# Optimization experiments

Measured on AMD Instinct MI355X. Metric: run time of the kernel, lower is better.

Reference implementation:

```python
import jax, jax.numpy as jnp
import numpy as np

B, S, E, H, NE, TOPK = 8, 1024, 768, 12, 8, 2
F = 4 * E
DH = E // H

def _ln(x, g, b, eps=1e-5):
    m = jnp.mean(x, axis=-1, keepdims=True)
    v = jnp.mean((x - m) ** 2, axis=-1, keepdims=True)
    return (x - m) / jnp.sqrt(v + eps) * g + b

def _expert(x, lg, lb, w1, b1, w2, b2):
    # Expert: LayerNorm -> Linear(E,4E) -> GELU(exact) -> Linear(4E,E); dropout is identity in eval
    h = _ln(x, lg, lb)
    h = jax.nn.gelu(h @ w1.T + b1, approximate=False)
    return h @ w2.T + b2

def setup_inputs():
    key = jax.random.key(0)
    ks = jax.random.split(key, 16)
    rn = lambda k, shape, s=0.02: jax.random.normal(k, shape, jnp.float32) * s
    return {
        'x': jax.random.normal(ks[0], (B, S, E), jnp.float32),
        'modality_type': jax.random.randint(ks[1], (B, S), 0, 2).astype(jnp.int32),
        'norm1_g': jnp.ones((E,), jnp.float32), 'norm1_b': jnp.zeros((E,), jnp.float32),
        'norm2_g': jnp.ones((E,), jnp.float32), 'norm2_b': jnp.zeros((E,), jnp.float32),
        'in_proj_w': rn(ks[2], (3 * E, E)), 'in_proj_b': jnp.zeros((3 * E,), jnp.float32),
        'out_proj_w': rn(ks[3], (E, E)), 'out_proj_b': jnp.zeros((E,), jnp.float32),
        'router_w': rn(ks[4], (NE, E)), 'router_b': jnp.zeros((NE,), jnp.float32),
        'spec_ln_g': jnp.ones((3, E), jnp.float32), 'spec_ln_b': jnp.zeros((3, E), jnp.float32),
        'spec_w1': rn(ks[5], (3, F, E)), 'spec_b1': jnp.zeros((3, F), jnp.float32),
        'spec_w2': rn(ks[6], (3, E, F)), 'spec_b2': jnp.zeros((3, E), jnp.float32),
        'gen_ln_g': jnp.ones((NE, E), jnp.float32), 'gen_ln_b': jnp.zeros((NE, E), jnp.float32),
        'gen_w1': rn(ks[7], (NE, F, E)), 'gen_b1': jnp.zeros((NE, F), jnp.float32),
        'gen_w2': rn(ks[8], (NE, E, F)), 'gen_b2': jnp.zeros((NE, E), jnp.float32),
    }

def _forward(x, modality_type, norm1_g, norm1_b, norm2_g, norm2_b, in_proj_w, in_proj_b,
             out_proj_w, out_proj_b, router_w, router_b,
             spec_ln_g, spec_ln_b, spec_w1, spec_b1, spec_w2, spec_b2,
             gen_ln_g, gen_ln_b, gen_w1, gen_b1, gen_w2, gen_b2):
    # --- self-attention block (pre-norm + residual), matches nn.MultiheadAttention ---
    residual = x
    xn = _ln(x, norm1_g, norm1_b)
    qkv = xn @ in_proj_w.T + in_proj_b                          # [B,S,3E]
    q, k, v = jnp.split(qkv, 3, axis=-1)
    q = q.reshape(B, S, H, DH); k = k.reshape(B, S, H, DH); v = v.reshape(B, S, H, DH)
    scores = jnp.einsum('bqhd,bkhd->bhqk', q, k) / jnp.sqrt(jnp.float32(DH))
    attn = jax.nn.softmax(scores, axis=-1)
    ctx = jnp.einsum('bhqk,bkhd->bqhd', attn, v).reshape(B, S, E)
    x = residual + (ctx @ out_proj_w.T + out_proj_b)

    # --- MoE block (pre-norm + residual) ---
    residual = x
    xn = _ln(x, norm2_g, norm2_b)
    expert_out = _expert(xn, spec_ln_g[0], spec_ln_b[0], spec_w1[0], spec_b1[0], spec_w2[0], spec_b2[0])
    # modality experts: vision on tokens with type==0, text on type==1 (not a fusion layer)
    vmask = (modality_type == 0).astype(xn.dtype)[..., None]
    tmask = (modality_type == 1).astype(xn.dtype)[..., None]
    expert_out = expert_out + vmask * _expert(xn, spec_ln_g[1], spec_ln_b[1], spec_w1[1], spec_b1[1], spec_w2[1], spec_b2[1])
    expert_out = expert_out + tmask * _expert(xn, spec_ln_g[2], spec_ln_b[2], spec_w1[2], spec_b1[2], spec_w2[2], spec_b2[2])

    # --- router: softmax -> top_k -> renormalize over top_k ---
    logits = xn @ router_w.T + router_b                         # [B,S,NE]
    probs = jax.nn.softmax(logits, axis=-1)
    topk_probs, topk_idx = jax.lax.top_k(probs, TOPK)
    topk_w = jax.nn.softmax(topk_probs, axis=-1)                # [B,S,TOPK]

    # --- dispatch/combine: per-expert combine coefficient; experts are per-token so
    # dense masked compute is mathematically identical to the torch gather/scatter loop ---
    for e in range(NE):
        coef = jnp.sum(topk_w * (topk_idx == e), axis=-1)[..., None]   # [B,S,1]
        expert_out = expert_out + coef * _expert(xn, gen_ln_g[e], gen_ln_b[e], gen_w1[e], gen_b1[e], gen_w2[e], gen_b2[e])

    return residual + expert_out

def reference(x, modality_type, norm1_g, norm1_b, norm2_g, norm2_b, in_proj_w, in_proj_b,
              out_proj_w, out_proj_b, router_w, router_b,
              spec_ln_g, spec_ln_b, spec_w1, spec_b1, spec_w2, spec_b2,
              gen_ln_g, gen_ln_b, gen_w1, gen_b1, gen_w2, gen_b2):
    return _forward(x, modality_type, norm1_g, norm1_b, norm2_g, norm2_b, in_proj_w, in_proj_b,
                    out_proj_w, out_proj_b, router_w, router_b,
                    spec_ln_g, spec_ln_b, spec_w1, spec_b1, spec_w2, spec_b2,
                    gen_ln_g, gen_ln_b, gen_w1, gen_b1, gen_w2, gen_b2)
```

## Files before the change

kernel.cpp:

```cpp
#include <hip/hip_runtime.h>
#include <cstdint>

#define NTOK 8192
#define EDIM 768
#define FDIM 3072

using bf16x8 = __attribute__((ext_vector_type(8))) __bf16;
using f32x4  = __attribute__((ext_vector_type(4))) float;

__device__ __forceinline__ float b2f(ushort u){ union{uint32_t i; float f;} v; v.i = ((uint32_t)u)<<16; return v.f; }
__device__ __forceinline__ ushort f2b(float f){ union{float f; uint32_t i;} v; v.f=f; uint32_t r = v.i + 0x7fffu + ((v.i>>16)&1u); return (ushort)(r>>16); }
__device__ __forceinline__ float gelu_f(float v){
  float c = v*(1.5957691216f + 0.0713548162726f*v*v);
  return v / (1.f + __expf(-c));
}
__device__ __forceinline__ void gload16(const ushort* g, ushort* l){
  __builtin_amdgcn_global_load_lds((const __attribute__((address_space(1))) void*)g,
                                   (__attribute__((address_space(3))) void*)l, 16, 0, 0);
}

__global__ __launch_bounds__(256) void conv_w(const float* w0,const float* w1,const float* w2,
                                              const float* w3,const float* w4,const float* w5,
                                              const float* slg, const float* glg,
                                              ushort* pool)
{
  size_t idx4 = (size_t)blockIdx.x*256 + threadIdx.x;
  size_t e = idx4*4;
  const float* src; size_t base; int region;
  if      (e <  1769472u){src=w0;base=0;        region=0;}
  else if (e <  2359296u){src=w1;base=1769472u; region=1;}
  else if (e <  9437184u){src=w2;base=2359296u; region=2;}
  else if (e < 16515072u){src=w3;base=9437184u; region=3;}
  else if (e < 35389440u){src=w4;base=16515072u;region=4;}
  else                   {src=w5;base=35389440u;region=5;}
  size_t within = e - base;
  f32x4 f = *(const f32x4*)(src + within);
  if (region==2){
    int ex = (int)(within/2359296u); int col = (int)(within%768u);
    f32x4 g = *(const f32x4*)(slg + ex*768 + col);
    f[0]*=g[0]; f[1]*=g[1]; f[2]*=g[2]; f[3]*=g[3];
  } else if (region==4){
    int ex = (int)(within/2359296u); int col = (int)(within%768u);
    f32x4 g = *(const f32x4*)(glg + ex*768 + col);
    f[0]*=g[0]; f[1]*=g[1]; f[2]*=g[2]; f[3]*=g[3];
  }
  ushort4 u; u.x=f2b(f[0]); u.y=f2b(f[1]); u.z=f2b(f[2]); u.w=f2b(f[3]);
  *(ushort4*)(pool+e) = u;
}

__global__ __launch_bounds__(256) void b1fold_k(const float* __restrict__ sw1, const float* __restrict__ gw1,
                                                const float* __restrict__ sb1, const float* __restrict__ gb1,
                                                const float* __restrict__ slb, const float* __restrict__ glb,
                                                float* __restrict__ b1p)
{
  int j = blockIdx.x*4 + (threadIdx.x>>6);
  int lane = threadIdx.x & 63;
  int je = j / FDIM, f = j % FDIM;
  const float* wrow = (je<3) ? sw1 + ((size_t)je*FDIM + f)*EDIM : gw1 + ((size_t)(je-3)*FDIM + f)*EDIM;
  const float* lb   = (je<3) ? slb + (size_t)je*EDIM : glb + (size_t)(je-3)*EDIM;
  float s = 0.f;
  #pragma unroll
  for (int i=0;i<12;i++){ int d = lane + 64*i; s += wrow[d]*lb[d]; }
  #pragma unroll
  for (int o=32;o>0;o>>=1) s += __shfl_xor(s,o);
  if (lane==0){
    float base = (je<3) ? sb1[je*FDIM+f] : gb1[(je-3)*FDIM+f];
    b1p[j] = base + s;
  }
}

__global__ __launch_bounds__(256) void out_init(const float* __restrict__ x, const float* __restrict__ bo,
                                                float* __restrict__ out)
{
  size_t i = ((size_t)blockIdx.x*256 + threadIdx.x)*4;
  int col = (int)(i % EDIM);
  f32x4 xv = *(const f32x4*)(x+i);
  f32x4 bv = *(const f32x4*)(bo+col);
  f32x4 r = { xv[0]+bv[0], xv[1]+bv[1], xv[2]+bv[2], xv[3]+bv[3] };
  *(f32x4*)(out+i) = r;
}

__global__ __launch_bounds__(256) void ln1_k(const float* __restrict__ x, const float* __restrict__ g,
                                             const float* __restrict__ b, ushort* __restrict__ out)
{
  int w = blockIdx.x*4 + (threadIdx.x>>6);
  int lane = threadIdx.x & 63;
  const float* xr = x + (size_t)w*EDIM;
  float v[12]; float s=0.f, s2=0.f;
  #pragma unroll
  for (int i=0;i<12;i++){ v[i]=xr[lane+64*i]; s+=v[i]; s2+=v[i]*v[i]; }
  #pragma unroll
  for (int o=32;o>0;o>>=1){ s += __shfl_xor(s,o); s2 += __shfl_xor(s2,o); }
  float mu = s*(1.f/768.f);
  float rs = rsqrtf(s2*(1.f/768.f) - mu*mu + 1e-5f);
  ushort* op = out + (size_t)w*EDIM;
  #pragma unroll
  for (int i=0;i<12;i++){ int d=lane+64*i; op[d] = f2b((v[i]-mu)*rs*g[d] + b[d]); }
}

__global__ __launch_bounds__(256) void lnr_k(const float* __restrict__ x1, const float* __restrict__ g2,
                                             const float* __restrict__ b2, const float* __restrict__ rw,
                                             const float* __restrict__ rbv,
                                             ushort* __restrict__ z, float* __restrict__ coef)
{
  int w = blockIdx.x*4 + (threadIdx.x>>6);
  int lane = threadIdx.x & 63;
  const float* xr = x1 + (size_t)w*EDIM;
  float v[12]; float s=0.f, s2=0.f;
  #pragma unroll
  for (int i=0;i<12;i++){ v[i]=xr[lane+64*i]; s+=v[i]; s2+=v[i]*v[i]; }
  #pragma unroll
  for (int o=32;o>0;o>>=1){ s += __shfl_xor(s,o); s2 += __shfl_xor(s2,o); }
  float mu = s*(1.f/768.f);
  float rs = rsqrtf(s2*(1.f/768.f) - mu*mu + 1e-5f);
  float xn[12]; s=0.f; s2=0.f;
  #pragma unroll
  for (int i=0;i<12;i++){ int d=lane+64*i; xn[i]=(v[i]-mu)*rs*g2[d]+b2[d]; s+=xn[i]; s2+=xn[i]*xn[i]; }
  float pl[8] = {0.f,0.f,0.f,0.f,0.f,0.f,0.f,0.f};
  #pragma unroll
  for (int i=0;i<12;i++){
    int d=lane+64*i; float xv=xn[i];
    #pragma unroll
    for (int e=0;e<8;e++) pl[e] += xv * rw[e*EDIM + d];
  }
  #pragma unroll
  for (int o=32;o>0;o>>=1){ s += __shfl_xor(s,o); s2 += __shfl_xor(s2,o); }
  float mu2 = s*(1.f/768.f);
  float rs2 = rsqrtf(s2*(1.f/768.f) - mu2*mu2 + 1e-5f);
  ushort* op = z + (size_t)w*EDIM;
  #pragma unroll
  for (int i=0;i<12;i++){ int d=lane+64*i; op[d] = f2b((xn[i]-mu2)*rs2); }
  #pragma unroll
  for (int e=0;e<8;e++){
    #pragma unroll
    for (int o=32;o>0;o>>=1) pl[e] += __shfl_xor(pl[e], o);
  }
  float lgt[8]; float mx = -1e30f;
  #pragma unroll
  for (int e=0;e<8;e++){ lgt[e]=pl[e]+rbv[e]; mx = fmaxf(mx, lgt[e]); }
  float p[8]; float den=0.f;
  #pragma unroll
  for (int e=0;e<8;e++){ p[e]=__expf(lgt[e]-mx); den+=p[e]; }
  float inv = 1.f/den;
  #pragma unroll
  for (int e=0;e<8;e++) p[e]*=inv;
  int i1=0;
  #pragma unroll
  for (int e=1;e<8;e++) if (p[e]>p[i1]) i1=e;
  int i2=(i1==0)?1:0;
  #pragma unroll
  for (int e=0;e<8;e++){ if (e==i1) continue; if (p[e]>p[i2]) i2=e; }
  float w1 = 1.f/(1.f+__expf(p[i2]-p[i1]));
  float w2 = 1.f - w1;
  if (lane < 8){
    float c = (lane==i1)? w1 : ((lane==i2)? w2 : 0.f);
    coef[(size_t)w*8 + lane] = c;
  }
}

__global__ __launch_bounds__(256) void build_lists(const int* __restrict__ mt, const float* __restrict__ coef,
                                                   ushort* __restrict__ lists, ushort* __restrict__ inv,
                                                   int* __restrict__ cnt)
{
  const int job = blockIdx.x;
  ushort* list = lists + (size_t)job*NTOK;
  __shared__ int wsum[4];
  int base = 0;
  const int lane = threadIdx.x & 63, wv = threadIdx.x >> 6;
  for (int c0=0; c0<NTOK; c0+=256){
    int t = c0 + threadIdx.x;
    bool flag;
    if (job==0)      flag = (mt[t]==0);
    else if (job==1) flag = (mt[t]==1);
    else             flag = (coef[(size_t)t*8 + (job-2)] != 0.0f);
    unsigned long long bal = __ballot(flag);
    int pre = __popcll(bal & ((1ull<<lane)-1ull));
    if (lane==0) wsum[wv] = __popcll(bal);
    __syncthreads();
    int off = base + pre;
    for (int k=0;k<wv;k++) off += wsum[k];
    int tot = wsum[0]+wsum[1]+wsum[2]+wsum[3];
    if (flag){ list[off] = (ushort)t; inv[(size_t)job*NTOK + t] = (ushort)off; }
    base += tot;
    __syncthreads();
  }
  if (threadIdx.x==0){ cnt[job+1] = base; if (job==0) cnt[0] = NTOK; }
}

__global__ __launch_bounds__(256) void gather_k(const float* __restrict__ coef, const int* __restrict__ mt,
                                                const ushort* __restrict__ inv, const int* __restrict__ cnt,
                                                const ushort* __restrict__ outC, float* __restrict__ out,
                                                int phase)
{
  int t = blockIdx.x*4 + (threadIdx.x>>6);
  int lane = threadIdx.x & 63;
  int r0, r1; float c0=1.f, c1=1.f;
  if (phase==0){
    r0 = t;
    int m = mt[t];
    r1 = NTOK + (m ? cnt[1] : 0) + (int)inv[(size_t)m*NTOK + t];
  } else {
    int found=0; int rr[2]={0,0}; float cc[2]={0.f,0.f}; int base=0;
    #pragma unroll
    for (int e=0;e<8;e++){
      float ce = coef[(size_t)t*8+e];
      if (ce != 0.f && found<2){ rr[found]=base+(int)inv[(size_t)(2+e)*NTOK + t]; cc[found]=ce; found++; }
      base += cnt[3+e];
    }
    r0=rr[0]; r1=rr[1]; c0=cc[0]; c1=cc[1];
  }
  const ushort* pa = outC + (size_t)r0*EDIM;
  const ushort* pb = outC + (size_t)r1*EDIM;
  float* po = out + (size_t)t*EDIM;
  #pragma unroll
  for (int i=0;i<3;i++){
    int d = lane*4 + 256*i;
    ushort4 ua = *(const ushort4*)(pa+d);
    ushort4 ub = *(const ushort4*)(pb+d);
    f32x4 o = *(f32x4*)(po+d);
    o[0] += c0*b2f(ua.x) + c1*b2f(ub.x);
    o[1] += c0*b2f(ua.y) + c1*b2f(ub.y);
    o[2] += c0*b2f(ua.z) + c1*b2f(ub.z);
    o[3] += c0*b2f(ua.w) + c1*b2f(ub.w);
    *(f32x4*)(po+d) = o;
  }
}

struct GemmArgs {
  const ushort* A; const ushort* B;
  const float* bias;
  ushort* outBF;
  int K, ldc;
};

__global__ __launch_bounds__(256) void gemm_k(GemmArgs g)
{
  const int mb = blockIdx.x, nb = blockIdx.y;
  __shared__ __align__(1024) ushort As[128*32];
  __shared__ __align__(1024) ushort Bs[128*32];
  const int tid = threadIdx.x;
  const int lane = tid & 63, w = tid >> 6;
  const int seg = lane & 3;
  const int lrow = w*16 + (lane>>2);
  const int p = (lane>>3)&3;
  ushort* ldsA0 = As + (size_t)w*512;
  ushort* ldsA1 = As + (size_t)(w+4)*512;
  ushort* ldsB0 = Bs + (size_t)w*512;
  ushort* ldsB1 = Bs + (size_t)(w+4)*512;
  const int KK = g.K;
  const ushort* pA0 = g.A + (size_t)(mb*128 + lrow)*KK + (seg^p)*8;
  const ushort* pA1 = pA0 + (size_t)64*KK;
  const ushort* pB0 = g.B + (size_t)(nb*128 + lrow)*KK + (seg^p)*8;
  const ushort* pB1 = pB0 + (size_t)64*KK;
  const int nst = KK >> 5;
  f32x4 acc[4][4];
  #pragma unroll
  for (int m=0;m<4;m++)
    #pragma unroll
    for (int n=0;n<4;n++) acc[m][n] = (f32x4){0.f,0.f,0.f,0.f};
  const int fr = lane & 15, fq = lane >> 4;
  const int pr = (fr>>1)&3;
  const int so = (fq^pr)*8;
  const int rb_ = (w>>1)*64, cb_ = (w&1)*64;
  for (int kt=0; kt<nst; ++kt){
    __syncthreads();
    gload16(pA0, ldsA0); gload16(pA1, ldsA1);
    gload16(pB0, ldsB0); gload16(pB1, ldsB1);
    pA0 += 32; pA1 += 32; pB0 += 32; pB1 += 32;
    __syncthreads();
    bf16x8 af[4], bfr[4];
    #pragma unroll
    for (int m=0;m<4;m++) af[m]  = *(const bf16x8*)&As[(rb_ + m*16 + fr)*32 + so];
    #pragma unroll
    for (int n=0;n<4;n++) bfr[n] = *(const bf16x8*)&Bs[(cb_ + n*16 + fr)*32 + so];
    #pragma unroll
    for (int m=0;m<4;m++)
      #pragma unroll
      for (int n=0;n<4;n++)
        acc[m][n] = __builtin_amdgcn_mfma_f32_16x16x32_bf16(af[m], bfr[n], acc[m][n], 0, 0, 0);
  }
  #pragma unroll
  for (int m=0;m<4;m++){
    #pragma unroll
    for (int j=0;j<4;j++){
      const int row = mb*128 + rb_ + m*16 + fq*4 + j;
      #pragma unroll
      for (int n=0;n<4;n++){
        const int col = nb*128 + cb_ + n*16 + fr;
        g.outBF[(size_t)row*g.ldc + col] = f2b(acc[m][n][j] + g.bias[col]);
      }
    }
  }
}

struct FArgs {
  const ushort* z; ushort* hidden; const ushort* ctx; const ushort* wo;
  float* out; ushort* outC;
  const ushort* lists; const ushort* inv; const int* cnt; const float* coef;
  const ushort* sw1; const ushort* gw1; const ushort* sw2; const ushort* gw2;
  const float* b1p; const float* sb2; const float* gb2;
  int jobBase; int compact; int mode;
};

__device__ __forceinline__ size_t job_hoff(const FArgs& a, int job){
  size_t h = 0;
  if (a.compact){
    if (job==1) h = NTOK;
    else if (job==2) h = NTOK + (size_t)a.cnt[1];
    else if (job>=3){ for (int k=3;k<job;k++) h += (size_t)a.cnt[k]; }
  }
  return h;
}

__global__ __launch_bounds__(256) void ffn1_k(FArgs a)
{
  const int job = a.jobBase + blockIdx.z;
  const int cntj = (job==0) ? NTOK : a.cnt[job];
  const int mb = blockIdx.x, nb = blockIdx.y;
  if (mb*128 >= cntj) return;
  const ushort* list = (job==0) ? nullptr : a.lists + (size_t)(job-1)*NTOK;
  const ushort* B = (job<3) ? a.sw1+(size_t)job*FDIM*EDIM : a.gw1+(size_t)(job-3)*FDIM*EDIM;
  const float* bias = a.b1p + (size_t)job*FDIM;
  const size_t hoff = job_hoff(a, job);
  __shared__ __align__(1024) ushort As[128*32];
  __shared__ __align__(1024) ushort Bs[128*32];
  const int tid = threadIdx.x;
  const int lane = tid & 63, w = tid >> 6;
  const int seg = lane & 3;
  const int lrow = w*16 + (lane>>2);
  const int p = (lane>>3)&3;
  ushort* ldsA0 = As + (size_t)w*512;
  ushort* ldsA1 = As + (size_t)(w+4)*512;
  ushort* ldsB0 = Bs + (size_t)w*512;
  ushort* ldsB1 = Bs + (size_t)(w+4)*512;
  const int r0 = mb*128 + lrow, r1 = r0 + 64;
  const int tA0 = list ? (int)list[min(r0,cntj-1)] : min(r0,cntj-1);
  const int tA1 = list ? (int)list[min(r1,cntj-1)] : min(r1,cntj-1);
  const ushort* pA0 = a.z + (size_t)tA0*EDIM + (seg^p)*8;
  const ushort* pA1 = a.z + (size_t)tA1*EDIM + (seg^p)*8;
  const ushort* pB0 = B + (size_t)(nb*128 + lrow)*EDIM + (seg^p)*8;
  const ushort* pB1 = pB0 + (size_t)64*EDIM;
  f32x4 acc[4][4];
  #pragma unroll
  for (int m=0;m<4;m++)
    #pragma unroll
    for (int n=0;n<4;n++) acc[m][n] = (f32x4){0.f,0.f,0.f,0.f};
  const int fr = lane & 15, fq = lane >> 4;
  const int pr = (fr>>1)&3;
  const int so = (fq^pr)*8;
  const int rb_ = (w>>1)*64, cb_ = (w&1)*64;
  for (int kt=0; kt<24; ++kt){
    __syncthreads();
    gload16(pA0, ldsA0); gload16(pA1, ldsA1);
    gload16(pB0, ldsB0); gload16(pB1, ldsB1);
    pA0 += 32; pA1 += 32; pB0 += 32; pB1 += 32;
    __syncthreads();
    bf16x8 af[4], bfr[4];
    #pragma unroll
    for (int m=0;m<4;m++) af[m]  = *(const bf16x8*)&As[(rb_ + m*16 + fr)*32 + so];
    #pragma unroll
    for (int n=0;n<4;n++) bfr[n] = *(const bf16x8*)&Bs[(cb_ + n*16 + fr)*32 + so];
    #pragma unroll
    for (int m=0;m<4;m++)
      #pragma unroll
      for (int n=0;n<4;n++)
        acc[m][n] = __builtin_amdgcn_mfma_f32_16x16x32_bf16(af[m], bfr[n], acc[m][n], 0, 0, 0);
  }
  #pragma unroll
  for (int m=0;m<4;m++){
    #pragma unroll
    for (int j=0;j<4;j++){
      const int row = mb*128 + rb_ + m*16 + fq*4 + j;
      if (row < cntj){
        #pragma unroll
        for (int n=0;n<4;n++){
          const int col = nb*128 + cb_ + n*16 + fr;
          a.hidden[(hoff+row)*FDIM + col] = f2b(gelu_f(acc[m][n][j] + bias[col]));
        }
      }
    }
  }
}

__global__ __launch_bounds__(256) void ffn2_k(FArgs a)
{
  const bool op = (a.jobBase < 0);
  const int job = op ? -1 : a.jobBase + blockIdx.z;
  const int cntj = op ? NTOK : ((job==0) ? NTOK : a.cnt[job]);
  const int mb = blockIdx.x, nb = blockIdx.y;
  if (mb*64 >= cntj) return;
  const ushort* list = (op || job==0) ? nullptr : a.lists + (size_t)(job-1)*NTOK;
  const ushort* Abase; int lda; const ushort* B; const float* bias = nullptr;
  const float* coefp = nullptr; int eidx = 0;
  if (op){ Abase = a.ctx; lda = EDIM; B = a.wo; }
  else {
    lda = FDIM;
    Abase = a.hidden + job_hoff(a, job)*FDIM;
    if (job<3){ B=a.sw2+(size_t)job*(size_t)EDIM*FDIM; bias=a.sb2+(size_t)job*EDIM; }
    else { eidx=job-3; B=a.gw2+(size_t)eidx*(size_t)EDIM*FDIM; bias=a.gb2+(size_t)eidx*EDIM; coefp=a.coef; }
  }
  const size_t hoff = op ? 0 : job_hoff(a, job);
  const int nst = lda >> 5;
  __shared__ __align__(1024) ushort As[64*32];
  __shared__ __align__(1024) ushort Bs[128*32];
  const int tid = threadIdx.x;
  const int lane = tid & 63, w = tid >> 6;
  const int seg = lane & 3;
  const int lrow = w*16 + (lane>>2);
  const int p = (lane>>3)&3;
  ushort* ldsA  = As + (size_t)w*512;
  ushort* ldsB0 = Bs + (size_t)w*512;
  ushort* ldsB1 = Bs + (size_t)(w+4)*512;
  const int r0 = mb*64 + lrow;
  const ushort* pA  = Abase + (size_t)min(r0,cntj-1)*lda + (seg^p)*8;
  const ushort* pB0 = B + (size_t)(nb*128 + lrow)*lda + (seg^p)*8;
  const ushort* pB1 = pB0 + (size_t)64*lda;
  f32x4 acc[4][2];
  #pragma unroll
  for (int m=0;m<4;m++)
    #pragma unroll
    for (int n=0;n<2;n++) acc[m][n] = (f32x4){0.f,0.f,0.f,0.f};
  const int fr = lane & 15, fq = lane >> 4;
  const int pr = (fr>>1)&3;
  const int so = (fq^pr)*8;
  const int cb_ = w*32;
  for (int kt=0; kt<nst; ++kt){
    __syncthreads();
    gload16(pA, ldsA);
    gload16(pB0, ldsB0); gload16(pB1, ldsB1);
    pA += 32; pB0 += 32; pB1 += 32;
    __syncthreads();
    bf16x8 af[4], bfr[2];
    #pragma unroll
    for (int m=0;m<4;m++) af[m]  = *(const bf16x8*)&As[(m*16 + fr)*32 + so];
    #pragma unroll
    for (int n=0;n<2;n++) bfr[n] = *(const bf16x8*)&Bs[(cb_ + n*16 + fr)*32 + so];
    #pragma unroll
    for (int m=0;m<4;m++)
      #pragma unroll
      for (int n=0;n<2;n++)
        acc[m][n] = __builtin_amdgcn_mfma_f32_16x16x32_bf16(af[m], bfr[n], acc[m][n], 0, 0, 0);
  }
  #pragma unroll
  for (int m=0;m<4;m++){
    #pragma unroll
    for (int j=0;j<4;j++){
      const int row = mb*64 + m*16 + fq*4 + j;
      if (row < cntj){
        #pragma unroll
        for (int n=0;n<2;n++){
          const int col = nb*128 + cb_ + n*16 + fr;
          float v = acc[m][n][j];
          if (op){
            a.out[(size_t)row*EDIM + col] += v;
          } else if (a.mode==1){
            a.outC[(hoff+row)*EDIM + col] = f2b(v + bias[col]);
          } else {
            const int tok = list ? (int)list[row] : row;
            const float c = coefp ? coefp[(size_t)tok*8 + eidx] : 1.0f;
            atomicAdd(&a.out[(size_t)tok*EDIM + col], c*(v + bias[col]));
          }
        }
      }
    }
  }
}

__global__ __launch_bounds__(256) void attn_k(const ushort* __restrict__ qkv, ushort* __restrict__ ctx)
{
  const int qb = blockIdx.x, bh = blockIdx.y;
  const int b = bh/12, h = bh%12;
  const int tid = threadIdx.x;
  const int lane = tid & 63, w = tid >> 6;
  const int fr = lane & 15, fq = lane >> 4;
  __shared__ __align__(16) ushort Ks[4096];
  __shared__ __align__(16) ushort Vts[4096];
  __shared__ __align__(16) ushort Ps[4096];
  const size_t tokq = (size_t)b*1024 + (size_t)qb*64;

  bf16x8 qf[2];
  {
    const ushort* qp = qkv + (tokq + w*16 + fr)*2304 + h*64 + fq*8;
    qf[0] = *(const bf16x8*)(qp);
    qf[1] = *(const bf16x8*)(qp + 32);
  }
  f32x4 o[4];
  #pragma unroll
  for (int nt=0;nt<4;nt++) o[nt] = (f32x4){0.f,0.f,0.f,0.f};
  float m[4] = {-1e30f,-1e30f,-1e30f,-1e30f};
  float l[4] = {0.f,0.f,0.f,0.f};

  const int skr = tid>>3, skc = (tid&7)*8;
  const int svd = (tid&15)*4, svk = (tid>>4)*4;

  for (int kt=0; kt<16; ++kt){
    __syncthreads();
    const size_t tokk = (size_t)b*1024 + (size_t)kt*64;
    #pragma unroll
    for (int pp=0;pp<2;pp++){
      int row = skr + pp*32;
      uint4 kq = *(const uint4*)(qkv + (tokk+row)*2304 + 768 + h*64 + skc);
      *(uint4*)&Ks[row*64 + (skc ^ ((row&7)<<3))] = kq;
    }
    {
      union { ushort4 v4[4]; ushort s[16]; } tv;
      #pragma unroll
      for (int i=0;i<4;i++)
        tv.v4[i] = *(const ushort4*)(qkv + (tokk+svk+i)*2304 + 1536 + h*64 + svd);
      #pragma unroll
      for (int j=0;j<4;j++){
        ushort4 tj; tj.x=tv.s[j]; tj.y=tv.s[4+j]; tj.z=tv.s[8+j]; tj.w=tv.s[12+j];
        int dr = svd + j;
        *(ushort4*)&Vts[dr*64 + (svk ^ ((dr&7)<<3))] = tj;
      }
    }
    __syncthreads();
    f32x4 s[4];
    #pragma unroll
    for (int nt=0;nt<4;nt++){
      s[nt] = (f32x4){0.f,0.f,0.f,0.f};
      int kr = nt*16 + fr;
      const ushort* kb = &Ks[kr*64];
      int sw = (kr&7)<<3;
      bf16x8 k0 = *(const bf16x8*)&kb[(fq*8) ^ sw];
      bf16x8 k1 = *(const bf16x8*)&kb[(fq*8+32) ^ sw];
      s[nt] = __builtin_amdgcn_mfma_f32_16x16x32_bf16(qf[0], k0, s[nt], 0,0,0);
      s[nt] = __builtin_amdgcn_mfma_f32_16x16x32_bf16(qf[1], k1, s[nt], 0,0,0);
    }
    float a_[4], pr[4][4];
    #pragma unroll
    for (int j=0;j<4;j++){
      float mx = fmaxf(fmaxf(s[0][j],s[1][j]), fmaxf(s[2][j],s[3][j])) * 0.125f;
      mx = fmaxf(mx, __shfl_xor(mx,1));
      mx = fmaxf(mx, __shfl_xor(mx,2));
      mx = fmaxf(mx, __shfl_xor(mx,4));
      mx = fmaxf(mx, __shfl_xor(mx,8));
      float mn = fmaxf(m[j], mx);
      float aa = __expf(m[j] - mn);
      m[j] = mn; a_[j] = aa;
      float ss = 0.f;
      #pragma unroll
      for (int nt=0;nt<4;nt++){
        float pv = __expf(s[nt][j]*0.125f - mn);
        pr[nt][j] = pv; ss += pv;
      }
      ss += __shfl_xor(ss,1);
      ss += __shfl_xor(ss,2);
      ss += __shfl_xor(ss,4);
      ss += __shfl_xor(ss,8);
      l[j] = l[j]*aa + ss;
    }
    #pragma unroll
    for (int nt=0;nt<4;nt++){
      #pragma unroll
      for (int j=0;j<4;j++){
        int row = fq*4 + j;
        Ps[w*1024 + row*64 + ((nt*16+fr) ^ ((row&7)<<3))] = f2b(pr[nt][j]);
        o[nt][j] *= a_[j];
      }
    }
    #pragma unroll
    for (int ks=0; ks<2; ++ks){
      int kvo = ks*32 + fq*8;
      bf16x8 pf = *(const bf16x8*)&Ps[w*1024 + fr*64 + (kvo ^ ((fr&7)<<3))];
      #pragma unroll
      for (int nt=0;nt<4;nt++){
        int dr = nt*16 + fr;
        bf16x8 vf = *(const bf16x8*)&Vts[dr*64 + (kvo ^ ((dr&7)<<3))];
        o[nt] = __builtin_amdgcn_mfma_f32_16x16x32_bf16(pf, vf, o[nt], 0,0,0);
      }
    }
  }
  float inv[4];
  #pragma unroll
  for (int j=0;j<4;j++) inv[j] = 1.f/l[j];
  ushort* cp = ctx + (tokq + w*16)*768 + h*64;
  #pragma unroll
  for (int nt=0;nt<4;nt++){
    #pragma unroll
    for (int j=0;j<4;j++){
      cp[(size_t)(fq*4+j)*768 + nt*16 + fr] = f2b(o[nt][j]*inv[j]);
    }
  }
}

#define OFF_POOL   0u
#define OFF_Z      108527616u
#define OFF_COEF   121110528u
#define OFF_LISTS  121372672u
#define OFF_INV    121536512u
#define OFF_CNT    121700352u
#define OFF_B1P    121700608u
#define OFF_QKV    121835776u
#define OFF_CTX    159584512u
#define OFF_XN1    172167424u
#define WS_GROUPED 222499072u
#define OFF_OUTC   222499072u
#define WS_BIG     247664896u

extern "C" void kernel_launch(void* const* d_in, const int* in_sizes, int n_in,
                              void* d_out, int out_size, void* d_ws, size_t ws_size,
                              hipStream_t stream)
{
  const float* x    = (const float*)d_in[0];
  const int*   mt   = (const int*)d_in[1];
  const float* n1g  = (const float*)d_in[2];
  const float* n1b  = (const float*)d_in[3];
  const float* n2g  = (const float*)d_in[4];
  const float* n2b  = (const float*)d_in[5];
  const float* wqkv = (const float*)d_in[6];
  const float* bqkv = (const float*)d_in[7];
  const float* wo   = (const float*)d_in[8];
  const float* bo   = (const float*)d_in[9];
  const float* rw   = (const float*)d_in[10];
  const float* rb   = (const float*)d_in[11];
  const float* slg  = (const float*)d_in[12];
  const float* slb  = (const float*)d_in[13];
  const float* sw1  = (const float*)d_in[14];
  const float* sb1  = (const float*)d_in[15];
  const float* sw2  = (const float*)d_in[16];
  const float* sb2  = (const float*)d_in[17];
  const float* glg  = (const float*)d_in[18];
  const float* glb  = (const float*)d_in[19];
  const float* gw1  = (const float*)d_in[20];
  const float* gb1  = (const float*)d_in[21];
  const float* gw2  = (const float*)d_in[22];
  const float* gb2  = (const float*)d_in[23];
  float* out = (float*)d_out;
  char* ws = (char*)d_ws;

  ushort* pool  = (ushort*)(ws + OFF_POOL);
  ushort* z     = (ushort*)(ws + OFF_Z);
  float*  coef  = (float*) (ws + OFF_COEF);
  ushort* lists = (ushort*)(ws + OFF_LISTS);
  ushort* invp  = (ushort*)(ws + OFF_INV);
  int*    cnt   = (int*)   (ws + OFF_CNT);
  float*  b1p   = (float*) (ws + OFF_B1P);
  ushort* qkv   = (ushort*)(ws + OFF_QKV);
  ushort* ctx   = (ushort*)(ws + OFF_CTX);
  ushort* xn1   = (ushort*)(ws + OFF_XN1);
  ushort* hidden= (ushort*)(ws + OFF_QKV);
  ushort* outC  = (ushort*)(ws + OFF_OUTC);

  ushort* pWqkv = pool + 0;
  ushort* pWo   = pool + 1769472;
  ushort* pSw1  = pool + 2359296;
  ushort* pSw2  = pool + 9437184;
  ushort* pGw1  = pool + 16515072;
  ushort* pGw2  = pool + 35389440;

  const int tier = (ws_size >= (size_t)WS_BIG) ? 2 : ((ws_size >= (size_t)WS_GROUPED) ? 1 : 0);

  conv_w<<<52992, 256, 0, stream>>>(wqkv, wo, sw1, sw2, gw1, gw2, slg, glg, pool);
  b1fold_k<<<8448, 256, 0, stream>>>(sw1, gw1, sb1, gb1, slb, glb, b1p);
  ln1_k<<<2048, 256, 0, stream>>>(x, n1g, n1b, xn1);
  { GemmArgs a{}; a.A=xn1; a.B=pWqkv; a.bias=bqkv; a.outBF=qkv; a.K=768; a.ldc=2304;
    gemm_k<<<dim3(64,18),256,0,stream>>>(a); }
  attn_k<<<dim3(16,96),256,0,stream>>>(qkv, ctx);
  out_init<<<6144,256,0,stream>>>(x, bo, out);

  FArgs fa{};
  fa.z=z; fa.hidden=hidden; fa.ctx=ctx; fa.wo=pWo; fa.out=out; fa.outC=outC;
  fa.lists=lists; fa.inv=invp; fa.cnt=cnt; fa.coef=coef;
  fa.sw1=pSw1; fa.gw1=pGw1; fa.sw2=pSw2; fa.gw2=pGw2;
  fa.b1p=b1p; fa.sb2=sb2; fa.gb2=gb2;

  { FArgs a = fa; a.jobBase = -1; a.compact = 0; a.mode = 0;
    ffn2_k<<<dim3(128,6,1),256,0,stream>>>(a); }

  lnr_k<<<2048,256,0,stream>>>(out, n2g, n2b, rw, rb, z, coef);
  build_lists<<<10,256,0,stream>>>(mt, coef, lists, invp, cnt);

  if (tier==2){
    { FArgs a = fa; a.jobBase = 0; a.compact = 1; a.mode = 1;
      ffn1_k<<<dim3(64,24,3),256,0,stream>>>(a);
      ffn2_k<<<dim3(128,6,3),256,0,stream>>>(a); }
    gather_k<<<2048,256,0,stream>>>(coef, mt, invp, cnt, outC, out, 0);
    { FArgs a = fa; a.jobBase = 3; a.compact = 1; a.mode = 1;
      ffn1_k<<<dim3(64,24,8),256,0,stream>>>(a);
      ffn2_k<<<dim3(128,6,8),256,0,stream>>>(a); }
    gather_k<<<2048,256,0,stream>>>(coef, mt, invp, cnt, outC, out, 1);
  } else if (tier==1){
    { FArgs a = fa; a.jobBase = 0; a.compact = 1; a.mode = 0;
      ffn1_k<<<dim3(64,24,3),256,0,stream>>>(a);
      ffn2_k<<<dim3(128,6,3),256,0,stream>>>(a); }
    { FArgs a = fa; a.jobBase = 3; a.compact = 1; a.mode = 0;
      ffn1_k<<<dim3(64,24,8),256,0,stream>>>(a);
      ffn2_k<<<dim3(128,6,8),256,0,stream>>>(a); }
  } else {
    for (int j=0;j<11;j++){
      FArgs a = fa; a.jobBase = j; a.compact = 0; a.mode = 0;
      ffn1_k<<<dim3(64,24,1),256,0,stream>>>(a);
      ffn2_k<<<dim3(128,6,1),256,0,stream>>>(a);
    }
  }
}
```

Before: 1.092 ms.

## Double-buffer LDS tiles in GEMM and FFN kernels to overlap loads with MFMA

```diff
diff --git a/kernel.cpp b/kernel.cpp
--- a/kernel.cpp
+++ b/kernel.cpp
@@ -236,17 +236,14 @@
 __global__ __launch_bounds__(256) void gemm_k(GemmArgs g)
 {
   const int mb = blockIdx.x, nb = blockIdx.y;
-  __shared__ __align__(1024) ushort As[128*32];
-  __shared__ __align__(1024) ushort Bs[128*32];
+  __shared__ __align__(1024) ushort As[2*128*32];
+  __shared__ __align__(1024) ushort Bs[2*128*32];
   const int tid = threadIdx.x;
   const int lane = tid & 63, w = tid >> 6;
   const int seg = lane & 3;
   const int lrow = w*16 + (lane>>2);
   const int p = (lane>>3)&3;
-  ushort* ldsA0 = As + (size_t)w*512;
-  ushort* ldsA1 = As + (size_t)(w+4)*512;
-  ushort* ldsB0 = Bs + (size_t)w*512;
-  ushort* ldsB1 = Bs + (size_t)(w+4)*512;
+  const int dstA0 = w*512, dstA1 = (w+4)*512;
   const int KK = g.K;
   const ushort* pA0 = g.A + (size_t)(mb*128 + lrow)*KK + (seg^p)*8;
   const ushort* pA1 = pA0 + (size_t)64*KK;
@@ -262,22 +259,32 @@
   const int pr = (fr>>1)&3;
   const int so = (fq^pr)*8;
   const int rb_ = (w>>1)*64, cb_ = (w&1)*64;
+  gload16(pA0, As+dstA0); gload16(pA1, As+dstA1);
+  gload16(pB0, Bs+dstA0); gload16(pB1, Bs+dstA1);
+  pA0 += 32; pA1 += 32; pB0 += 32; pB1 += 32;
+  __syncthreads();
+  int cur = 0;
   for (int kt=0; kt<nst; ++kt){
-    __syncthreads();
-    gload16(pA0, ldsA0); gload16(pA1, ldsA1);
-    gload16(pB0, ldsB0); gload16(pB1, ldsB1);
-    pA0 += 32; pA1 += 32; pB0 += 32; pB1 += 32;
-    __syncthreads();
+    if (kt+1 < nst){
+      int nxt = (cur^1)*4096;
+      gload16(pA0, As+nxt+dstA0); gload16(pA1, As+nxt+dstA1);
+      gload16(pB0, Bs+nxt+dstA0); gload16(pB1, Bs+nxt+dstA1);
+      pA0 += 32; pA1 += 32; pB0 += 32; pB1 += 32;
+    }
+    const ushort* Ab = As + cur*4096;
+    const ushort* Bb = Bs + cur*4096;
     bf16x8 af[4], bfr[4];
     #pragma unroll
-    for (int m=0;m<4;m++) af[m]  = *(const bf16x8*)&As[(rb_ + m*16 + fr)*32 + so];
-    #pragma unroll
-    for (int n=0;n<4;n++) bfr[n] = *(const bf16x8*)&Bs[(cb_ + n*16 + fr)*32 + so];
+    for (int m=0;m<4;m++) af[m]  = *(const bf16x8*)&Ab[(rb_ + m*16 + fr)*32 + so];
+    #pragma unroll
+    for (int n=0;n<4;n++) bfr[n] = *(const bf16x8*)&Bb[(cb_ + n*16 + fr)*32 + so];
     #pragma unroll
     for (int m=0;m<4;m++)
       #pragma unroll
       for (int n=0;n<4;n++)
         acc[m][n] = __builtin_amdgcn_mfma_f32_16x16x32_bf16(af[m], bfr[n], acc[m][n], 0, 0, 0);
+    __syncthreads();
+    cur ^= 1;
   }
   #pragma unroll
   for (int m=0;m<4;m++){
@@ -322,17 +329,14 @@
   const ushort* B = (job<3) ? a.sw1+(size_t)job*FDIM*EDIM : a.gw1+(size_t)(job-3)*FDIM*EDIM;
   const float* bias = a.b1p + (size_t)job*FDIM;
   const size_t hoff = job_hoff(a, job);
-  __shared__ __align__(1024) ushort As[128*32];
-  __shared__ __align__(1024) ushort Bs[128*32];
+  __shared__ __align__(1024) ushort As[2*128*32];
+  __shared__ __align__(1024) ushort Bs[2*128*32];
   const int tid = threadIdx.x;
   const int lane = tid & 63, w = tid >> 6;
   const int seg = lane & 3;
   const int lrow = w*16 + (lane>>2);
   const int p = (lane>>3)&3;
-  ushort* ldsA0 = As + (size_t)w*512;
-  ushort* ldsA1 = As + (size_t)(w+4)*512;
-  ushort* ldsB0 = Bs + (size_t)w*512;
-  ushort* ldsB1 = Bs + (size_t)(w+4)*512;
+  const int dstA0 = w*512, dstA1 = (w+4)*512;
   const int r0 = mb*128 + lrow, r1 = r0 + 64;
   const int tA0 = list ? (int)list[min(r0,cntj-1)] : min(r0,cntj-1);
   const int tA1 = list ? (int)list[min(r1,cntj-1)] : min(r1,cntj-1);
@@ -349,22 +353,32 @@
   const int pr = (fr>>1)&3;
   const int so = (fq^pr)*8;
   const int rb_ = (w>>1)*64, cb_ = (w&1)*64;
+  gload16(pA0, As+dstA0); gload16(pA1, As+dstA1);
+  gload16(pB0, Bs+dstA0); gload16(pB1, Bs+dstA1);
+  pA0 += 32; pA1 += 32; pB0 += 32; pB1 += 32;
+  __syncthreads();
+  int cur = 0;
   for (int kt=0; kt<24; ++kt){
-    __syncthreads();
-    gload16(pA0, ldsA0); gload16(pA1, ldsA1);
-    gload16(pB0, ldsB0); gload16(pB1, ldsB1);
-    pA0 += 32; pA1 += 32; pB0 += 32; pB1 += 32;
-    __syncthreads();
+    if (kt+1 < 24){
+      int nxt = (cur^1)*4096;
+      gload16(pA0, As+nxt+dstA0); gload16(pA1, As+nxt+dstA1);
+      gload16(pB0, Bs+nxt+dstA0); gload16(pB1, Bs+nxt+dstA1);
+      pA0 += 32; pA1 += 32; pB0 += 32; pB1 += 32;
+    }
+    const ushort* Ab = As + cur*4096;
+    const ushort* Bb = Bs + cur*4096;
     bf16x8 af[4], bfr[4];
     #pragma unroll
-    for (int m=0;m<4;m++) af[m]  = *(const bf16x8*)&As[(rb_ + m*16 + fr)*32 + so];
-    #pragma unroll
-    for (int n=0;n<4;n++) bfr[n] = *(const bf16x8*)&Bs[(cb_ + n*16 + fr)*32 + so];
+    for (int m=0;m<4;m++) af[m]  = *(const bf16x8*)&Ab[(rb_ + m*16 + fr)*32 + so];
+    #pragma unroll
+    for (int n=0;n<4;n++) bfr[n] = *(const bf16x8*)&Bb[(cb_ + n*16 + fr)*32 + so];
     #pragma unroll
     for (int m=0;m<4;m++)
       #pragma unroll
       for (int n=0;n<4;n++)
         acc[m][n] = __builtin_amdgcn_mfma_f32_16x16x32_bf16(af[m], bfr[n], acc[m][n], 0, 0, 0);
+    __syncthreads();
+    cur ^= 1;
   }
   #pragma unroll
   for (int m=0;m<4;m++){
@@ -401,16 +415,14 @@
   }
   const size_t hoff = op ? 0 : job_hoff(a, job);
   const int nst = lda >> 5;
-  __shared__ __align__(1024) ushort As[64*32];
-  __shared__ __align__(1024) ushort Bs[128*32];
+  __shared__ __align__(1024) ushort As[2*64*32];
+  __shared__ __align__(1024) ushort Bs[2*128*32];
   const int tid = threadIdx.x;
   const int lane = tid & 63, w = tid >> 6;
   const int seg = lane & 3;
   const int lrow = w*16 + (lane>>2);
   const int p = (lane>>3)&3;
-  ushort* ldsA  = As + (size_t)w*512;
-  ushort* ldsB0 = Bs + (size_t)w*512;
-  ushort* ldsB1 = Bs + (size_t)(w+4)*512;
+  const int dstA0 = w*512, dstA1 = (w+4)*512;
   const int r0 = mb*64 + lrow;
   const ushort* pA  = Abase + (size_t)min(r0,cntj-1)*lda + (seg^p)*8;
   const ushort* pB0 = B + (size_t)(nb*128 + lrow)*lda + (seg^p)*8;
@@ -424,22 +436,31 @@
   const int pr = (fr>>1)&3;
   const int so = (fq^pr)*8;
   const int cb_ = w*32;
+  gload16(pA, As+dstA0);
+  gload16(pB0, Bs+dstA0); gload16(pB1, Bs+dstA1);
+  pA += 32; pB0 += 32; pB1 += 32;
+  __syncthreads();
+  int cur = 0;
   for (int kt=0; kt<nst; ++kt){
-    __syncthreads();
-    gload16(pA, ldsA);
-    gload16(pB0, ldsB0); gload16(pB1, ldsB1);
-    pA += 32; pB0 += 32; pB1 += 32;
-    __syncthreads();
+    if (kt+1 < nst){
+      gload16(pA, As+(cur^1)*2048+dstA0);
+      gload16(pB0, Bs+(cur^1)*4096+dstA0); gload16(pB1, Bs+(cur^1)*4096+dstA1);
+      pA += 32; pB0 += 32; pB1 += 32;
+    }
+    const ushort* Ab = As + cur*2048;
+    const ushort* Bb = Bs + cur*4096;
     bf16x8 af[4], bfr[2];
     #pragma unroll
-    for (int m=0;m<4;m++) af[m]  = *(const bf16x8*)&As[(m*16 + fr)*32 + so];
-    #pragma unroll
-    for (int n=0;n<2;n++) bfr[n] = *(const bf16x8*)&Bs[(cb_ + n*16 + fr)*32 + so];
+    for (int m=0;m<4;m++) af[m]  = *(const bf16x8*)&Ab[(m*16 + fr)*32 + so];
+    #pragma unroll
+    for (int n=0;n<2;n++) bfr[n] = *(const bf16x8*)&Bb[(cb_ + n*16 + fr)*32 + so];
     #pragma unroll
     for (int m=0;m<4;m++)
       #pragma unroll
       for (int n=0;n<2;n++)
         acc[m][n] = __builtin_amdgcn_mfma_f32_16x16x32_bf16(af[m], bfr[n], acc[m][n], 0, 0, 0);
+    __syncthreads();
+    cur ^= 1;
   }
   #pragma unroll
   for (int m=0;m<4;m++){
```

After: 1.114 ms. 1.02x slower.
